# Optimization experiments

Hardware: AMD Instinct MI355X
Metric: run time of the kernel (lower is better)

## Reference

```python
import jax, jax.numpy as jnp
import numpy as np

DIM = 1024
NUM_HEADS = 16
HEAD_DIM = DIM // NUM_HEADS
SCALE = HEAD_DIM ** -0.5


def setup_inputs() -> dict:
    key = jax.random.key(0)
    ks = jax.random.split(key, 7)
    b, n = 2, 2048
    x = jax.random.normal(ks[0], (b, n, DIM), dtype=jnp.float32)
    s = DIM ** -0.5
    Wq = jax.random.normal(ks[1], (DIM, DIM), dtype=jnp.float32) * s
    bq = jax.random.normal(ks[2], (DIM,), dtype=jnp.float32) * 0.01
    Wk = jax.random.normal(ks[3], (DIM, DIM), dtype=jnp.float32) * s
    bk = jax.random.normal(ks[4], (DIM,), dtype=jnp.float32) * 0.01
    Wv = jax.random.normal(ks[5], (DIM, DIM), dtype=jnp.float32) * s
    bv = jax.random.normal(ks[6], (DIM,), dtype=jnp.float32) * 0.01
    return {"x": x, "Wq": Wq, "bq": bq, "Wk": Wk, "bk": bk, "Wv": Wv, "bv": bv}


def reference(x, Wq, bq, Wk, bk, Wv, bv):
    b, n, _ = x.shape
    # Linear projections (torch Linear: x @ W.T + b; here W stored as [in, out])
    q = x @ Wq + bq
    k = x @ Wk + bk
    v = x @ Wv + bv
    # split heads: [b, n, h*d] -> [b, h, n, d]
    split = lambda t: t.reshape(b, n, NUM_HEADS, HEAD_DIM).transpose(0, 2, 1, 3)
    q, k, v = split(q), split(k), split(v)
    sim = jnp.einsum('bhid,bhjd->bhij', q, k) * SCALE
    attn = jax.nn.softmax(sim, axis=-1)
    out = jnp.einsum('bhij,bhjd->bhid', attn, v)
    return out.transpose(0, 2, 1, 3).reshape(b, n, DIM)
```

## Files before the change

kernel.cpp:

```cpp
#include <hip/hip_runtime.h>
#include <cstdint>
#include <cstddef>

#define NB    2
#define SEQ   2048
#define DIMC  1024
#define NH    16
#define HDIM  64
#define MROWS (NB*SEQ)
#define NFEAT (3*DIMC)
#define KVBLK 64
#define NT    (SEQ/KVBLK)

typedef _Float16 half8 __attribute__((ext_vector_type(8)));
typedef _Float16 half4 __attribute__((ext_vector_type(4)));
typedef _Float16 half2v __attribute__((ext_vector_type(2)));
typedef __fp16   fp16x2 __attribute__((ext_vector_type(2)));
typedef float    f32x4 __attribute__((ext_vector_type(4)));

typedef const __attribute__((address_space(1))) void* gas_ptr;
typedef __attribute__((address_space(3))) void*       las_ptr;

__device__ __forceinline__ void gload_lds16(const void* g, void* l) {
    __builtin_amdgcn_global_load_lds((gas_ptr)g, (las_ptr)l, 16, 0, 0);
}

__device__ __forceinline__ int swz4(int r) { return (r ^ (r >> 2)) & 3; }

__device__ __forceinline__ float fast_exp2(float x) {
    float r;
    asm("v_exp_f32 %0, %1" : "=v"(r) : "v"(x));
    return r;
}

__device__ __forceinline__ half2v pk_f16(float a, float b) {
    fp16x2 r = __builtin_amdgcn_cvt_pkrtz(a, b);
    return __builtin_bit_cast(half2v, r);
}

__global__ __launch_bounds__(256) void k_convert_x(const float* __restrict__ x,
                                                   _Float16* __restrict__ x16) {
    int i = (blockIdx.x * 256 + threadIdx.x) * 4;
    float4 v = *reinterpret_cast<const float4*>(x + i);
    half4 h = { (_Float16)v.x, (_Float16)v.y, (_Float16)v.z, (_Float16)v.w };
    *reinterpret_cast<half4*>(x16 + i) = h;
}

__global__ __launch_bounds__(256) void k_transpose_w(const float* __restrict__ Wq,
                                                     const float* __restrict__ Wk,
                                                     const float* __restrict__ Wv,
                                                     _Float16* __restrict__ wt) {
    __shared__ float tile[64][65];
    const int bid  = blockIdx.x;
    const int midx = bid >> 8;
    const int t2   = bid & 255;
    const int i0   = (t2 >> 4) * 64;
    const int o0   = (t2 & 15) * 64;
    const float* W = (midx == 0) ? Wq : (midx == 1 ? Wk : Wv);
    const int tid  = threadIdx.x;
    #pragma unroll
    for (int p = 0; p < 4; ++p) {
        int id = p * 256 + tid;
        int r = id >> 4, c4 = (id & 15) * 4;
        float4 v = *reinterpret_cast<const float4*>(W + (size_t)(i0 + r) * DIMC + o0 + c4);
        tile[r][c4 + 0] = v.x; tile[r][c4 + 1] = v.y;
        tile[r][c4 + 2] = v.z; tile[r][c4 + 3] = v.w;
    }
    __syncthreads();
    #pragma unroll
    for (int p = 0; p < 4; ++p) {
        int id = p * 256 + tid;
        int oc = id >> 4, i4 = (id & 15) * 4;
        half4 h = { (_Float16)tile[i4 + 0][oc], (_Float16)tile[i4 + 1][oc],
                    (_Float16)tile[i4 + 2][oc], (_Float16)tile[i4 + 3][oc] };
        *reinterpret_cast<half4*>(wt + (size_t)(midx * DIMC + o0 + oc) * DIMC + i0 + i4) = h;
    }
}

__global__ __launch_bounds__(256) void k_qkv_gemm(
    const _Float16* __restrict__ x16, const _Float16* __restrict__ wt,
    const float* __restrict__ bq, const float* __restrict__ bk, const float* __restrict__ bv,
    _Float16* __restrict__ q16, _Float16* __restrict__ k16, _Float16* __restrict__ vt16)
{
    __shared__ __align__(16) char sraw[34816];
    const int tid = threadIdx.x;
    const int lane = tid & 63;
    const int w = tid >> 6, wm = w >> 1, wn = w & 1;
    const int lr = lane & 15, lg = lane >> 4;
    const int bn = blockIdx.x % (NFEAT / 128);
    const int bm = blockIdx.x / (NFEAT / 128);
    const int m0 = bm * 128, n0 = bn * 128;

    const f32x4 zero4 = {0.f, 0.f, 0.f, 0.f};
    f32x4 acc[4][4];
    #pragma unroll
    for (int i = 0; i < 4; ++i)
        #pragma unroll
        for (int j = 0; j < 4; ++j) acc[i][j] = zero4;

    auto stage = [&](int buf, int kt) {
        const int k0 = kt * 32;
        char* Adst = sraw + buf * 8192;
        char* Bdst = sraw + 16384 + buf * 8192;
        #pragma unroll
        for (int t = 0; t < 2; ++t) {
            int slot = t * 256 + tid;
            int row = slot >> 2, ch = slot & 3;
            int chg = ch ^ swz4(row);
            gload_lds16(x16 + (size_t)(m0 + row) * DIMC + k0 + chg * 8, Adst + slot * 16);
            gload_lds16(wt  + (size_t)(n0 + row) * DIMC + k0 + chg * 8, Bdst + slot * 16);
        }
    };

    stage(0, 0);
    for (int kt = 0; kt < DIMC / 32; ++kt) {
        __syncthreads();
        if (kt + 1 < DIMC / 32) stage((kt + 1) & 1, kt + 1);
        const char* Ab = sraw + (kt & 1) * 8192;
        const char* Bb = sraw + 16384 + (kt & 1) * 8192;
        half8 af[4], bf[4];
        #pragma unroll
        for (int mb = 0; mb < 4; ++mb) {
            int row = wm * 64 + mb * 16 + lr;
            af[mb] = *(const half8*)(Ab + row * 64 + ((lg ^ swz4(row)) << 4));
        }
        #pragma unroll
        for (int nb = 0; nb < 4; ++nb) {
            int col = wn * 64 + nb * 16 + lr;
            bf[nb] = *(const half8*)(Bb + col * 64 + ((lg ^ swz4(col)) << 4));
        }
        #pragma unroll
        for (int mb = 0; mb < 4; ++mb)
            #pragma unroll
            for (int nb = 0; nb < 4; ++nb)
                acc[mb][nb] = __builtin_amdgcn_mfma_f32_16x16x32_f16(af[mb], bf[nb], acc[mb][nb], 0, 0, 0);
    }

    const int sec = n0 >> 10;
    const float* bias = (sec == 0) ? bq : (sec == 1 ? bk : bv);
    const float scl = (sec == 0) ? 0.125f * 1.44269504088896f : 1.0f;
    float bfv[4];
    #pragma unroll
    for (int nb = 0; nb < 4; ++nb)
        bfv[nb] = bias[(n0 & 1023) + wn * 64 + nb * 16 + lr];

    if (sec < 2) {
        _Float16* dst = (sec == 0) ? q16 : k16;
        #pragma unroll
        for (int mb = 0; mb < 4; ++mb)
            #pragma unroll
            for (int i2 = 0; i2 < 4; ++i2) {
                int rg = m0 + wm * 64 + mb * 16 + lg * 4 + i2;
                int bb = rg >> 11, nn = rg & (SEQ - 1);
                #pragma unroll
                for (int nb = 0; nb < 4; ++nb) {
                    int f1 = (n0 & 1023) + wn * 64 + nb * 16 + lr;
                    int hh = f1 >> 6, dd = f1 & 63;
                    dst[((size_t)(bb * NH + hh) * SEQ + nn) * HDIM + dd] =
                        (_Float16)((acc[mb][nb][i2] + bfv[nb]) * scl);
                }
            }
    } else {
        __syncthreads();
        char* lt = sraw;
        #pragma unroll
        for (int mb = 0; mb < 4; ++mb)
            #pragma unroll
            for (int nb = 0; nb < 4; ++nb) {
                int c  = wn * 64 + nb * 16 + lr;
                int r0 = wm * 64 + mb * 16 + lg * 4;
                half4 hv = { (_Float16)(acc[mb][nb][0] + bfv[nb]),
                             (_Float16)(acc[mb][nb][1] + bfv[nb]),
                             (_Float16)(acc[mb][nb][2] + bfv[nb]),
                             (_Float16)(acc[mb][nb][3] + bfv[nb]) };
                *(half4*)(lt + c * 272 + r0 * 2) = hv;
            }
        __syncthreads();
        #pragma unroll
        for (int p = 0; p < 8; ++p) {
            int id = p * 256 + tid;
            int c = id >> 4, r8 = (id & 15) * 8;
            half8 hv = *(const half8*)(lt + c * 272 + r8 * 2);
            int f1 = (n0 & 1023) + c;
            int hh = f1 >> 6, dd = f1 & 63;
            int rg = m0 + r8;
            int bb = rg >> 11, nn = rg & (SEQ - 1);
            *(half8*)(vt16 + ((size_t)(bb * NH + hh) * HDIM + dd) * SEQ + nn) = hv;
        }
    }
}

__global__ __launch_bounds__(512) void k_attn(
    const _Float16* __restrict__ q16, const _Float16* __restrict__ k16,
    const _Float16* __restrict__ vt16, float* __restrict__ out)
{
    __shared__ __align__(16) char lds[49152];
    const int tid = threadIdx.x, lane = tid & 63, w = tid >> 6;
    const int lr = lane & 15, lg = lane >> 4;
    const int swz = (blockIdx.x & 7) * 64 + (blockIdx.x >> 3);
    const int bh = swz >> 4;
    const int qt = swz & 15;
    const int qrow0 = qt * 128 + w * 16;
    const _Float16* qh = q16 + (size_t)bh * SEQ * HDIM;
    const _Float16* kh = k16 + (size_t)bh * SEQ * HDIM;
    const _Float16* vh = vt16 + (size_t)bh * HDIM * SEQ;
    char* pl = lds + 32768 + w * 2048;
    const int rb = lr >> 3;

    const int srow = tid >> 3;
    const int scg  = (tid & 7) ^ (srow & 7);

    auto stageKV = [&](int buf, int j0) {
        gload_lds16(kh + (size_t)(j0 + srow) * HDIM + scg * 8,
                    lds + buf * 8192 + tid * 16);
        gload_lds16(vh + (size_t)srow * SEQ + j0 + scg * 8,
                    lds + 16384 + buf * 8192 + tid * 16);
    };

    half8 aq[2];
    #pragma unroll
    for (int kc = 0; kc < 2; ++kc)
        aq[kc] = *(const half8*)(qh + (size_t)(qrow0 + lr) * HDIM + kc * 32 + lg * 8);

    const f32x4 zero4 = {0.f, 0.f, 0.f, 0.f};
    f32x4 l4 = zero4;
    f32x4 oacc[4];
    #pragma unroll
    for (int i = 0; i < 4; ++i) oacc[i] = zero4;

    stageKV(0, 0);
    for (int t = 0; t < NT; ++t) {
        const int j0 = t * KVBLK;
        __syncthreads();
        if (t + 1 < NT) stageKV((t + 1) & 1, j0 + KVBLK);
        const char* Kb = lds + (t & 1) * 8192;
        const char* Vb = lds + 16384 + (t & 1) * 8192;

        f32x4 s[4];
        __builtin_amdgcn_s_setprio(1);
        #pragma unroll
        for (int jb = 0; jb < 4; ++jb) {
            int row = jb * 16 + lr;
            half8 k0 = *(const half8*)(Kb + row * 128 + (((0 + lg) ^ (row & 7)) << 4));
            half8 k1 = *(const half8*)(Kb + row * 128 + (((4 + lg) ^ (row & 7)) << 4));
            f32x4 sa = zero4;
            sa = __builtin_amdgcn_mfma_f32_16x16x32_f16(k0, aq[0], sa, 0, 0, 0);
            sa = __builtin_amdgcn_mfma_f32_16x16x32_f16(k1, aq[1], sa, 0, 0, 0);
            s[jb] = sa;
        }
        __builtin_amdgcn_s_setprio(0);

        half8 vf[4][2];
        #pragma unroll
        for (int db = 0; db < 4; ++db)
            #pragma unroll
            for (int kc = 0; kc < 2; ++kc) {
                int row = db * 16 + lr;
                vf[db][kc] = *(const half8*)(Vb + row * 128 + (((kc * 4 + lg) ^ (row & 7)) << 4));
            }

        #pragma unroll
        for (int jb = 0; jb < 4; ++jb) {
            #pragma unroll
            for (int i = 0; i < 4; ++i)
                s[jb][i] = fast_exp2(s[jb][i]);
            l4 += s[jb];
        }

        #pragma unroll
        for (int jb = 0; jb < 4; ++jb) {
            half2v w0 = pk_f16(s[jb][0], s[jb][1]);
            half2v w1 = pk_f16(s[jb][2], s[jb][3]);
            half4 pk = { w0.x, w0.y, w1.x, w1.y };
            *(half4*)(pl + lr * 128 + (((jb * 2 + (lg >> 1)) ^ (lr & 7)) << 4)
                      + (((lg & 1) ^ rb) << 3)) = pk;
        }
        asm volatile("s_waitcnt lgkmcnt(0)" ::: "memory");
        const char* prow = pl + lr * 128;
        half4 l0 = *(const half4*)(prow + (((0 + lg) ^ (lr & 7)) << 4) + (rb << 3));
        half4 h0 = *(const half4*)(prow + (((0 + lg) ^ (lr & 7)) << 4) + ((1 ^ rb) << 3));
        half4 l1 = *(const half4*)(prow + (((4 + lg) ^ (lr & 7)) << 4) + (rb << 3));
        half4 h1 = *(const half4*)(prow + (((4 + lg) ^ (lr & 7)) << 4) + ((1 ^ rb) << 3));
        half8 ap0 = { l0.x, l0.y, l0.z, l0.w, h0.x, h0.y, h0.z, h0.w };
        half8 ap1 = { l1.x, l1.y, l1.z, l1.w, h1.x, h1.y, h1.z, h1.w };
        __builtin_amdgcn_s_setprio(1);
        #pragma unroll
        for (int db = 0; db < 4; ++db) {
            oacc[db] = __builtin_amdgcn_mfma_f32_16x16x32_f16(ap0, vf[db][0], oacc[db], 0, 0, 0);
            oacc[db] = __builtin_amdgcn_mfma_f32_16x16x32_f16(ap1, vf[db][1], oacc[db], 0, 0, 0);
        }
        __builtin_amdgcn_s_setprio(0);
    }

    float l_i = (l4[0] + l4[1]) + (l4[2] + l4[3]);
    l_i += __shfl_xor(l_i, 16);
    l_i += __shfl_xor(l_i, 32);

    const int bb = bh >> 4, hh = bh & 15;
    float rlq[4];
    #pragma unroll
    for (int i = 0; i < 4; ++i)
        rlq[i] = 1.0f / __shfl(l_i, lg * 4 + i);
    #pragma unroll
    for (int db = 0; db < 4; ++db)
        #pragma unroll
        for (int i = 0; i < 4; ++i) {
            int nn = qrow0 + lg * 4 + i;
            out[((size_t)bb * SEQ + nn) * DIMC + hh * HDIM + db * 16 + lr] = oacc[db][i] * rlq[i];
        }
}

extern "C" void kernel_launch(void* const* d_in, const int* in_sizes, int n_in,
                              void* d_out, int out_size, void* d_ws, size_t ws_size,
                              hipStream_t stream)
{
    const float* x  = (const float*)d_in[0];
    const float* Wq = (const float*)d_in[1];
    const float* bq = (const float*)d_in[2];
    const float* Wk = (const float*)d_in[3];
    const float* bk = (const float*)d_in[4];
    const float* Wv = (const float*)d_in[5];
    const float* bv = (const float*)d_in[6];
    float* out = (float*)d_out;

    char* ws = (char*)d_ws;
    _Float16* x16  = (_Float16*)ws;
    _Float16* wt   = (_Float16*)(ws + ((size_t)8  << 20));
    _Float16* q16  = (_Float16*)(ws + ((size_t)14 << 20));
    _Float16* k16  = (_Float16*)(ws + ((size_t)22 << 20));
    _Float16* vt16 = (_Float16*)(ws + ((size_t)30 << 20));

    k_convert_x<<<MROWS * DIMC / 1024, 256, 0, stream>>>(x, x16);
    k_transpose_w<<<3 * 256, 256, 0, stream>>>(Wq, Wk, Wv, wt);
    k_qkv_gemm<<<(MROWS / 128) * (NFEAT / 128), 256, 0, stream>>>(x16, wt, bq, bk, bv,
                                                                  q16, k16, vt16);
    k_attn<<<32 * (SEQ / 128), 512, 0, stream>>>(q16, k16, vt16, out);
}
```

Measured before the change: 93.20 us.

## Process two 16-row query groups per wave in attention, halving block size

Each wave of the attention kernel now handles 32 query rows (two 16-row groups) instead of 16, so blocks shrink from 8 to 4 waves while still covering 128 query rows. K and V fragments loaded from LDS are reused across both groups, which halves LDS reads per MFMA and gives more independent MFMAs per wave to interleave. Each thread now issues two async loads per K/V tile. The cost is roughly double the accumulator and fragment registers per wave and fewer waves per block to hide latency.

```diff
diff --git a/kernel.cpp b/kernel.cpp
--- a/kernel.cpp
+++ b/kernel.cpp
@@ -190,7 +190,7 @@
     }
 }
 
-__global__ __launch_bounds__(512) void k_attn(
+__global__ __launch_bounds__(256) void k_attn(
     const _Float16* __restrict__ q16, const _Float16* __restrict__ k16,
     const _Float16* __restrict__ vt16, float* __restrict__ out)
 {
@@ -200,33 +200,40 @@
     const int swz = (blockIdx.x & 7) * 64 + (blockIdx.x >> 3);
     const int bh = swz >> 4;
     const int qt = swz & 15;
-    const int qrow0 = qt * 128 + w * 16;
+    const int qrow0 = qt * 128 + w * 32;
     const _Float16* qh = q16 + (size_t)bh * SEQ * HDIM;
     const _Float16* kh = k16 + (size_t)bh * SEQ * HDIM;
     const _Float16* vh = vt16 + (size_t)bh * HDIM * SEQ;
-    char* pl = lds + 32768 + w * 2048;
+    char* pl = lds + 32768 + w * 4096;
     const int rb = lr >> 3;
 
-    const int srow = tid >> 3;
-    const int scg  = (tid & 7) ^ (srow & 7);
-
     auto stageKV = [&](int buf, int j0) {
-        gload_lds16(kh + (size_t)(j0 + srow) * HDIM + scg * 8,
-                    lds + buf * 8192 + tid * 16);
-        gload_lds16(vh + (size_t)srow * SEQ + j0 + scg * 8,
-                    lds + 16384 + buf * 8192 + tid * 16);
+        #pragma unroll
+        for (int t = 0; t < 2; ++t) {
+            int slot = t * 256 + tid;
+            int row  = slot >> 3;
+            int chg  = (slot & 7) ^ (row & 7);
+            gload_lds16(kh + (size_t)(j0 + row) * HDIM + chg * 8,
+                        lds + buf * 8192 + slot * 16);
+            gload_lds16(vh + (size_t)row * SEQ + j0 + chg * 8,
+                        lds + 16384 + buf * 8192 + slot * 16);
+        }
     };
 
-    half8 aq[2];
-    #pragma unroll
-    for (int kc = 0; kc < 2; ++kc)
-        aq[kc] = *(const half8*)(qh + (size_t)(qrow0 + lr) * HDIM + kc * 32 + lg * 8);
+    half8 aq[2][2];
+    #pragma unroll
+    for (int g = 0; g < 2; ++g)
+        #pragma unroll
+        for (int kc = 0; kc < 2; ++kc)
+            aq[g][kc] = *(const half8*)(qh + (size_t)(qrow0 + g * 16 + lr) * HDIM + kc * 32 + lg * 8);
 
     const f32x4 zero4 = {0.f, 0.f, 0.f, 0.f};
-    f32x4 l4 = zero4;
-    f32x4 oacc[4];
-    #pragma unroll
-    for (int i = 0; i < 4; ++i) oacc[i] = zero4;
+    f32x4 l4[2] = { zero4, zero4 };
+    f32x4 oacc[2][4];
+    #pragma unroll
+    for (int g = 0; g < 2; ++g)
+        #pragma unroll
+        for (int i = 0; i < 4; ++i) oacc[g][i] = zero4;
 
     stageKV(0, 0);
     for (int t = 0; t < NT; ++t) {
@@ -236,17 +243,19 @@
         const char* Kb = lds + (t & 1) * 8192;
         const char* Vb = lds + 16384 + (t & 1) * 8192;
 
-        f32x4 s[4];
+        f32x4 s[2][4];
         __builtin_amdgcn_s_setprio(1);
         #pragma unroll
         for (int jb = 0; jb < 4; ++jb) {
             int row = jb * 16 + lr;
             half8 k0 = *(const half8*)(Kb + row * 128 + (((0 + lg) ^ (row & 7)) << 4));
             half8 k1 = *(const half8*)(Kb + row * 128 + (((4 + lg) ^ (row & 7)) << 4));
-            f32x4 sa = zero4;
-            sa = __builtin_amdgcn_mfma_f32_16x16x32_f16(k0, aq[0], sa, 0, 0, 0);
-            sa = __builtin_amdgcn_mfma_f32_16x16x32_f16(k1, aq[1], sa, 0, 0, 0);
-            s[jb] = sa;
+            f32x4 sa0 = zero4, sa1 = zero4;
+            sa0 = __builtin_amdgcn_mfma_f32_16x16x32_f16(k0, aq[0][0], sa0, 0, 0, 0);
+            sa1 = __builtin_amdgcn_mfma_f32_16x16x32_f16(k0, aq[1][0], sa1, 0, 0, 0);
+            sa0 = __builtin_amdgcn_mfma_f32_16x16x32_f16(k1, aq[0][1], sa0, 0, 0, 0);
+            sa1 = __builtin_amdgcn_mfma_f32_16x16x32_f16(k1, aq[1][1], sa1, 0, 0, 0);
+            s[0][jb] = sa0; s[1][jb] = sa1;
         }
         __builtin_amdgcn_s_setprio(0);
 
@@ -260,54 +269,63 @@
             }
 
         #pragma unroll
-        for (int jb = 0; jb < 4; ++jb) {
-            #pragma unroll
-            for (int i = 0; i < 4; ++i)
-                s[jb][i] = fast_exp2(s[jb][i]);
-            l4 += s[jb];
-        }
-
-        #pragma unroll
-        for (int jb = 0; jb < 4; ++jb) {
-            half2v w0 = pk_f16(s[jb][0], s[jb][1]);
-            half2v w1 = pk_f16(s[jb][2], s[jb][3]);
-            half4 pk = { w0.x, w0.y, w1.x, w1.y };
-            *(half4*)(pl + lr * 128 + (((jb * 2 + (lg >> 1)) ^ (lr & 7)) << 4)
-                      + (((lg & 1) ^ rb) << 3)) = pk;
+        for (int g = 0; g < 2; ++g) {
+            char* plg = pl + g * 2048;
+            #pragma unroll
+            for (int jb = 0; jb < 4; ++jb) {
+                #pragma unroll
+                for (int i = 0; i < 4; ++i)
+                    s[g][jb][i] = fast_exp2(s[g][jb][i]);
+                l4[g] += s[g][jb];
+                half2v w0 = pk_f16(s[g][jb][0], s[g][jb][1]);
+                half2v w1 = pk_f16(s[g][jb][2], s[g][jb][3]);
+                half4 pk = { w0.x, w0.y, w1.x, w1.y };
+                *(half4*)(plg + lr * 128 + (((jb * 2 + (lg >> 1)) ^ (lr & 7)) << 4)
+                          + (((lg & 1) ^ rb) << 3)) = pk;
+            }
         }
         asm volatile("s_waitcnt lgkmcnt(0)" ::: "memory");
-        const char* prow = pl + lr * 128;
-        half4 l0 = *(const half4*)(prow + (((0 + lg) ^ (lr & 7)) << 4) + (rb << 3));
-        half4 h0 = *(const half4*)(prow + (((0 + lg) ^ (lr & 7)) << 4) + ((1 ^ rb) << 3));
-        half4 l1 = *(const half4*)(prow + (((4 + lg) ^ (lr & 7)) << 4) + (rb << 3));
-        half4 h1 = *(const half4*)(prow + (((4 + lg) ^ (lr & 7)) << 4) + ((1 ^ rb) << 3));
-        half8 ap0 = { l0.x, l0.y, l0.z, l0.w, h0.x, h0.y, h0.z, h0.w };
-        half8 ap1 = { l1.x, l1.y, l1.z, l1.w, h1.x, h1.y, h1.z, h1.w };
+
+        half8 ap[2][2];
+        #pragma unroll
+        for (int g = 0; g < 2; ++g) {
+            const char* prow = pl + g * 2048 + lr * 128;
+            half4 l0 = *(const half4*)(prow + (((0 + lg) ^ (lr & 7)) << 4) + (rb << 3));
+            half4 h0 = *(const half4*)(prow + (((0 + lg) ^ (lr & 7)) << 4) + ((1 ^ rb) << 3));
+            half4 l1 = *(const half4*)(prow + (((4 + lg) ^ (lr & 7)) << 4) + (rb << 3));
+            half4 h1 = *(const half4*)(prow + (((4 + lg) ^ (lr & 7)) << 4) + ((1 ^ rb) << 3));
+            ap[g][0] = half8{ l0.x, l0.y, l0.z, l0.w, h0.x, h0.y, h0.z, h0.w };
+            ap[g][1] = half8{ l1.x, l1.y, l1.z, l1.w, h1.x, h1.y, h1.z, h1.w };
+        }
         __builtin_amdgcn_s_setprio(1);
         #pragma unroll
-        for (int db = 0; db < 4; ++db) {
-            oacc[db] = __builtin_amdgcn_mfma_f32_16x16x32_f16(ap0, vf[db][0], oacc[db], 0, 0, 0);
-            oacc[db] = __builtin_amdgcn_mfma_f32_16x16x32_f16(ap1, vf[db][1], oacc[db], 0, 0, 0);
-        }
+        for (int db = 0; db < 4; ++db)
+            #pragma unroll
+            for (int g = 0; g < 2; ++g) {
+                oacc[g][db] = __builtin_amdgcn_mfma_f32_16x16x32_f16(ap[g][0], vf[db][0], oacc[g][db], 0, 0, 0);
+                oacc[g][db] = __builtin_amdgcn_mfma_f32_16x16x32_f16(ap[g][1], vf[db][1], oacc[g][db], 0, 0, 0);
+            }
         __builtin_amdgcn_s_setprio(0);
     }
 
-    float l_i = (l4[0] + l4[1]) + (l4[2] + l4[3]);
-    l_i += __shfl_xor(l_i, 16);
-    l_i += __shfl_xor(l_i, 32);
-
     const int bb = bh >> 4, hh = bh & 15;
-    float rlq[4];
-    #pragma unroll
-    for (int i = 0; i < 4; ++i)
-        rlq[i] = 1.0f / __shfl(l_i, lg * 4 + i);
-    #pragma unroll
-    for (int db = 0; db < 4; ++db)
-        #pragma unroll
-        for (int i = 0; i < 4; ++i) {
-            int nn = qrow0 + lg * 4 + i;
-            out[((size_t)bb * SEQ + nn) * DIMC + hh * HDIM + db * 16 + lr] = oacc[db][i] * rlq[i];
-        }
+    #pragma unroll
+    for (int g = 0; g < 2; ++g) {
+        float l_i = (l4[g][0] + l4[g][1]) + (l4[g][2] + l4[g][3]);
+        l_i += __shfl_xor(l_i, 16);
+        l_i += __shfl_xor(l_i, 32);
+        float rlq[4];
+        #pragma unroll
+        for (int i = 0; i < 4; ++i)
+            rlq[i] = 1.0f / __shfl(l_i, lg * 4 + i);
+        #pragma unroll
+        for (int db = 0; db < 4; ++db)
+            #pragma unroll
+            for (int i = 0; i < 4; ++i) {
+                int nn = qrow0 + g * 16 + lg * 4 + i;
+                out[((size_t)bb * SEQ + nn) * DIMC + hh * HDIM + db * 16 + lr] = oacc[g][db][i] * rlq[i];
+            }
+    }
 }
 
 extern "C" void kernel_launch(void* const* d_in, const int* in_sizes, int n_in,
@@ -334,5 +352,5 @@
     k_transpose_w<<<3 * 256, 256, 0, stream>>>(Wq, Wk, Wv, wt);
     k_qkv_gemm<<<(MROWS / 128) * (NFEAT / 128), 256, 0, stream>>>(x16, wt, bq, bk, bv,
                                                                   q16, k16, vt16);
-    k_attn<<<32 * (SEQ / 128), 512, 0, stream>>>(q16, k16, vt16, out);
-}
+    k_attn<<<32 * (SEQ / 128), 256, 0, stream>>>(q16, k16, vt16, out);
+}
```

Result: slower. 99.42 us (+6.7%).
